# Optimization experiments

Hardware: AMD Instinct MI355X
Metric: run time of the kernel (lower is better)

Reference implementation:

```python
import jax, jax.numpy as jnp
import numpy as np
from jax import lax

# Module config (UOT_loss defaults): reg_m_l2=[5.0, 5.0], div='l2',
# detach_plan=True, use_uniform=False, marginal_match_dim=1.
REG_M1, REG_M2 = 5.0, 5.0
NUM_ITER = 1000      # POT mm_unbalanced default numItermax
STOP_THR = 1e-15     # POT default stopThr
EPS = 1e-16


def pairwise_sqeuclidean(x, y):
    # ot.dist default metric='sqeuclidean': M[i,j] = ||x_i - y_j||^2
    x2 = jnp.sum(x * x, axis=1)[:, None]
    y2 = jnp.sum(y * y, axis=1)[None, :]
    return jnp.maximum(x2 + y2 - 2.0 * (x @ y.T), 0.0)


def mm_unbalanced_l2(a, b, M):
    # POT ot.unbalanced.mm_unbalanced(a, b, M, [REG_M1, REG_M2], div='l2'), reg=0.
    G0 = a[:, None] * b[None, :]                       # [n, m] init plan
    K = jnp.maximum(REG_M1 * a[:, None] + REG_M2 * b[None, :] - M, 0.0)

    def cond(state):
        i, _, err = state
        return jnp.logical_and(i < NUM_ITER, err > STOP_THR)

    def body(state):
        i, G, _ = state
        Gd = (REG_M1 * jnp.sum(G, axis=1, keepdims=True)
              + REG_M2 * jnp.sum(G, axis=0, keepdims=True) + EPS)
        Gn = K * G / Gd
        err = jnp.sqrt(jnp.sum((Gn - G) ** 2))
        return i + 1, Gn, err

    _, G, _ = lax.while_loop(
        cond, body, (jnp.int32(0), G0, jnp.array(jnp.inf, G0.dtype)))
    return G


def setup_inputs() -> dict:
    key = jax.random.key(0)
    k1, k2, k3, k4 = jax.random.split(key, 4)
    n, m, d = 4096, 4096, 64
    source = jax.random.normal(k1, (n, d), jnp.float32)
    target = jax.random.normal(k2, (m, d), jnp.float32)
    mu = jax.random.uniform(k3, (n,), jnp.float32, minval=0.5, maxval=1.5)
    nu = jax.random.uniform(k4, (m,), jnp.float32, minval=0.5, maxval=1.5)
    mu = mu / jnp.sum(mu)
    nu = nu / jnp.sum(nu)
    return {"source": source, "target": target,
            "source_density": mu, "target_density": nu}


def reference(source, target, source_density, target_density):
    M = pairwise_sqeuclidean(source, target)           # [n, m]
    plan = mm_unbalanced_l2(source_density, target_density, M)
    ot_loss = jnp.sum(plan * M)
    # marginal_match_dim=1 -> row sums (transported source mass)
    marginal_transported = jnp.sum(plan, axis=1)
    marginal_loss = jnp.mean((marginal_transported - source_density) ** 2)
    return ot_loss, marginal_loss
```

## Files before the change

kernel.cpp:

```cpp
#include <hip/hip_runtime.h>


#define NV 4096
#define RM 5.0f
#define EPSF 1e-16f
#define STOP2 1e-30f
#define NITER 1000
#define MAGIC 0x5a17c0de
#define GRID_T 512

#define ERRT_OFF 0
#define ERRS_OFF 1024
#define OTP_OFF  2048
#define RSP_OFF  4096
#define CSP_OFF  135168
#define RS_OFF   266240
#define CS_OFF   270336
#define BMI_OFF  274432
#define CTL_OFF  275456
#define G_OFF    278528

typedef short bf16x8 __attribute__((ext_vector_type(8)));
typedef float f32x4  __attribute__((ext_vector_type(4)));
typedef unsigned short u16;

__device__ __forceinline__ float wave_sum_all(float v) {
  #pragma unroll
  for (int off = 1; off < 64; off <<= 1) v += __shfl_xor(v, off);
  return v;
}
__device__ __forceinline__ float wave_max_all(float v) {
  #pragma unroll
  for (int off = 1; off < 64; off <<= 1) v = fmaxf(v, __shfl_xor(v, off));
  return v;
}
__device__ __forceinline__ float wave_sum_dn(float v) {
  #pragma unroll
  for (int off = 32; off; off >>= 1) v += __shfl_down(v, off);
  return v;
}
__device__ __forceinline__ float dot64(const float* __restrict__ xr,
                                       const float* __restrict__ yr) {
  float d = 0.f;
  #pragma unroll 1
  for (int k = 0; k < 64; ++k) d = fmaf(xr[k], yr[k], d);
  return d;
}
__device__ __forceinline__ unsigned pack2(float x, float y) {
  return (__float_as_uint(x) >> 16) | (__float_as_uint(y) & 0xffff0000u);
}

__device__ void stage_panels(const float* __restrict__ X,
                             const float* __restrict__ Y,
                             int by, int bx,
                             u16 (*As)[72], u16 (*Bs)[72],
                             float* X2L, float* Y2L) {
  const int t = threadIdx.x;
  #pragma unroll
  for (int m = 0; m < 2; ++m) {
    const float* src = m ? (Y + (size_t)bx * 8192) : (X + (size_t)by * 8192);
    u16 (*dst)[72] = m ? Bs : As;
    float* nrm = m ? Y2L : X2L;
    #pragma unroll
    for (int it = 0; it < 8; ++it) {
      const int flat = t + it * 256;
      const int r = flat >> 4;
      const int c = (flat & 15) << 2;
      const float4 v = *(const float4*)(src + (size_t)flat * 4);
      float p = fmaf(v.x, v.x, fmaf(v.y, v.y, fmaf(v.z, v.z, v.w * v.w)));
      p += __shfl_xor(p, 1); p += __shfl_xor(p, 2);
      p += __shfl_xor(p, 4); p += __shfl_xor(p, 8);
      if ((t & 15) == 0) nrm[r] = p;
      uint2 w;
      w.x = pack2(v.x, v.y);
      w.y = pack2(v.z, v.w);
      *(uint2*)&dst[r][c] = w;
    }
  }
  __syncthreads();
}

__device__ void lds_dots(const u16 (*As)[72], const u16 (*Bs)[72],
                         int wr, int wc, int lane, f32x4 acc[4][4]) {
  const int lrow = lane & 15, lk8 = lane >> 4;
  #pragma unroll
  for (int i = 0; i < 4; ++i)
    #pragma unroll
    for (int j = 0; j < 4; ++j)
      acc[i][j] = (f32x4){0.f, 0.f, 0.f, 0.f};
  #pragma unroll
  for (int ks = 0; ks < 2; ++ks) {
    bf16x8 af[4], bg[4];
    #pragma unroll
    for (int f = 0; f < 4; ++f) {
      af[f] = *(const bf16x8*)&As[wr * 64 + f * 16 + lrow][ks * 32 + lk8 * 8];
      bg[f] = *(const bf16x8*)&Bs[wc * 64 + f * 16 + lrow][ks * 32 + lk8 * 8];
    }
    #pragma unroll
    for (int fr = 0; fr < 4; ++fr)
      #pragma unroll
      for (int fc = 0; fc < 4; ++fc)
        acc[fr][fc] = __builtin_amdgcn_mfma_f32_16x16x32_bf16(
            af[fr], bg[fc], acc[fr][fc], 0, 0, 0);
  }
}

__device__ __forceinline__ void gbar(int* ctl) {
  __threadfence();
  __syncthreads();
  if (threadIdx.x == 0) {
    while (__hip_atomic_load(&ctl[2], __ATOMIC_ACQUIRE,
                             __HIP_MEMORY_SCOPE_AGENT) != (int)MAGIC)
      __builtin_amdgcn_s_sleep(8);
    const int sense = __hip_atomic_load(&ctl[1], __ATOMIC_ACQUIRE,
                                        __HIP_MEMORY_SCOPE_AGENT);
    const int old = __hip_atomic_fetch_add(&ctl[0], 1, __ATOMIC_ACQ_REL,
                                           __HIP_MEMORY_SCOPE_AGENT);
    if (old == GRID_T - 1) {
      __hip_atomic_store(&ctl[0], 0, __ATOMIC_RELAXED, __HIP_MEMORY_SCOPE_AGENT);
      __hip_atomic_store(&ctl[1], sense ^ 1, __ATOMIC_RELEASE,
                         __HIP_MEMORY_SCOPE_AGENT);
    } else {
      while (__hip_atomic_load(&ctl[1], __ATOMIC_ACQUIRE,
                               __HIP_MEMORY_SCOPE_AGENT) == sense)
        __builtin_amdgcn_s_sleep(16);
    }
  }
  __syncthreads();
  __threadfence();
}

__global__ __launch_bounds__(256, 4) void k_main(
    const float* __restrict__ X, const float* __restrict__ Y,
    const float* __restrict__ a, const float* __restrict__ b,
    float* __restrict__ W) {
  __shared__ u16 As[128][72], Bs[128][72];
  __shared__ float X2L[128], Y2L[128];
  __shared__ float rcs[256], serr[4];
  __shared__ int s_nz;

  const int bid = blockIdx.x, tid = threadIdx.x;
  const int by = bid >> 5, bx = bid & 31;
  const int lane = tid & 63, wv = tid >> 6;
  const int wr = wv >> 1, wc = wv & 1;
  const int lrow = lane & 15, lk8 = lane >> 4;
  const int r0w = by * 128 + wr * 64;
  const int c0w = bx * 128 + wc * 64;
  float* Gp = W + G_OFF;
  int* bmi = (int*)(W + BMI_OFF);

  stage_panels(X, Y, by, bx, As, Bs, X2L, Y2L);

  f32x4 acc[4][4];
  lds_dots(As, Bs, wr, wc, lane, acc);

  const float av = a[r0w + lane];
  const float bv = b[c0w + lane];
  const float x2lv = X2L[wr * 64 + lane];
  const float y2lv = Y2L[wc * 64 + lane];
  const float amax = wave_max_all(av), bmax = wave_max_all(bv);
  const float x2m = wave_max_all(x2lv), y2m = wave_max_all(y2lv);
  const float Cw = RM * (amax + bmax) + 0.02f * sqrtf(x2m * y2m) + 0.05f;

  float x2r[16], y2c[4];
  #pragma unroll
  for (int fr = 0; fr < 4; ++fr)
    #pragma unroll
    for (int j = 0; j < 4; ++j)
      x2r[fr * 4 + j] = X2L[wr * 64 + fr * 16 + lk8 * 4 + j];
  #pragma unroll
  for (int fc = 0; fc < 4; ++fc)
    y2c[fc] = Y2L[wc * 64 + fc * 16 + lrow];

  float mmin = 3.4e38f;
  #pragma unroll
  for (int fr = 0; fr < 4; ++fr)
    #pragma unroll
    for (int j = 0; j < 4; ++j)
      #pragma unroll
      for (int fc = 0; fc < 4; ++fc)
        mmin = fminf(mmin,
                     fmaf(-2.f, acc[fr][fc][j], x2r[fr * 4 + j] + y2c[fc]));
  const bool wfast = (__ballot(mmin < Cw) == 0ull);

  if (tid == 0) s_nz = 0;
  rcs[tid] = 0.f;
  __syncthreads();

  if (wfast) {
    const float Ea = wave_sum_all(av * av);
    const float Eb = wave_sum_all(bv * bv);
    if (lane == 0) serr[wv] = Ea * Eb;
    #pragma unroll
    for (int fr = 0; fr < 4; ++fr)
      #pragma unroll
      for (int fc = 0; fc < 4; ++fc)
        acc[fr][fc] = (f32x4){0.f, 0.f, 0.f, 0.f};
  } else {
    float sa = 0.f, sb = 0.f;
    for (int i = lane; i < NV; i += 64) { sa += a[i]; sb += b[i]; }
    sa = wave_sum_all(sa); sb = wave_sum_all(sb);
    float bcf[4], gdc[4];
    #pragma unroll
    for (int fc = 0; fc < 4; ++fc) {
      bcf[fc] = __shfl(bv, fc * 16 + lrow);
      gdc[fc] = RM * bcf[fc] * sa;
    }
    float errp = 0.f; int nzl = 0;
    #pragma unroll
    for (int fr = 0; fr < 4; ++fr)
      #pragma unroll
      for (int j = 0; j < 4; ++j) {
        const int ridx = fr * 16 + lk8 * 4 + j;
        const float ar = __shfl(av, ridx);
        const float gdr = RM * ar * sb;
        const int grow = r0w + ridx;
        float rsum = 0.f;
        #pragma unroll
        for (int fc = 0; fc < 4; ++fc) {
          float Mv = fmaf(-2.f, acc[fr][fc][j], x2r[fr * 4 + j] + y2c[fc]);
          if (Mv < Cw) {
            const float dx = dot64(X + ((size_t)grow << 6),
                                   Y + ((size_t)(c0w + fc * 16 + lrow) << 6));
            Mv = x2r[fr * 4 + j] + y2c[fc] - 2.f * dx;
          }
          Mv = fmaxf(Mv, 0.f);
          const float Kv = fmaxf(RM * (ar + bcf[fc]) - Mv, 0.f);
          const float g0 = ar * bcf[fc];
          const float g = Kv * g0 / (gdr + gdc[fc] + EPSF);
          acc[fr][fc][j] = g;
          const float dl = g - g0;
          errp += dl * dl;
          nzl |= (g != 0.f);
          rsum += g;
        }
        atomicAdd(&rcs[wr * 64 + ridx], rsum);
      }
    #pragma unroll
    for (int fc = 0; fc < 4; ++fc) {
      float csum = 0.f;
      #pragma unroll
      for (int fr = 0; fr < 4; ++fr)
        #pragma unroll
        for (int j = 0; j < 4; ++j) csum += acc[fr][fc][j];
      atomicAdd(&rcs[128 + wc * 64 + fc * 16 + lrow], csum);
    }
    errp = wave_sum_all(errp);
    if (lane == 0) serr[wv] = errp;
    if (nzl) s_nz = 1;
  }
  __syncthreads();
  const int tilenz = s_nz;

  if (tilenz) {
    #pragma unroll
    for (int fr = 0; fr < 4; ++fr)
      #pragma unroll
      for (int j = 0; j < 4; ++j) {
        const int grow = r0w + fr * 16 + lk8 * 4 + j;
        #pragma unroll
        for (int fc = 0; fc < 4; ++fc)
          Gp[(size_t)grow * NV + c0w + fc * 16 + lrow] = acc[fr][fc][j];
      }
    if (tid < 128) W[RSP_OFF + (size_t)bid * 128 + tid] = rcs[tid];
    else           W[CSP_OFF + (size_t)bid * 128 + (tid - 128)] = rcs[tid];
  }
  if (tid == 0) {
    W[ERRT_OFF + bid] = serr[0] + serr[1] + serr[2] + serr[3];
    bmi[bid] = tilenz;
  }
}

__global__ __launch_bounds__(256, 2) void k_tail(
    const float* __restrict__ X, const float* __restrict__ Y,
    const float* __restrict__ a, const float* __restrict__ b,
    float* __restrict__ W, float* __restrict__ out) {
  __shared__ u16 As[128][72], Bs[128][72];
  __shared__ float X2L[128], Y2L[128];
  __shared__ float rcs[256], serr[4], sred[4];
  __shared__ int s_nz, s_any;

  const int bid = blockIdx.x, tid = threadIdx.x;
  const int lane = tid & 63, wv = tid >> 6;
  const int wr = wv >> 1, wc = wv & 1;
  const int lrow = lane & 15, lk8 = lane >> 4;
  float* Gp = W + G_OFF;
  int* bmi = (int*)(W + BMI_OFF);
  int* ctl = (int*)(W + CTL_OFF);

  if (bid == 0 && tid == 0) {
    __hip_atomic_store(&ctl[0], 0, __ATOMIC_RELAXED, __HIP_MEMORY_SCOPE_AGENT);
    __hip_atomic_store(&ctl[1], 0, __ATOMIC_RELAXED, __HIP_MEMORY_SCOPE_AGENT);
    __hip_atomic_store(&ctl[2], (int)MAGIC, __ATOMIC_RELEASE,
                       __HIP_MEMORY_SCOPE_AGENT);
  }

  int orv = 0;
  for (int i = tid; i < 1024; i += 256) orv |= bmi[i];
  if (tid == 0) s_any = 0;
  __syncthreads();
  if (orv) s_any = 1;
  __syncthreads();

  if (!s_any) {
    if (bid == 0) {
      float s = 0.f;
      for (int i = tid; i < NV; i += 256) { const float d = a[i]; s = fmaf(d, d, s); }
      s = wave_sum_dn(s);
      if (lane == 0) serr[wv] = s;
      __syncthreads();
      if (tid == 0) {
        out[0] = 0.f;
        out[1] = (serr[0] + serr[1] + serr[2] + serr[3]) * (1.0f / (float)NV);
      }
    }
    return;
  }

  const int t0 = bid, t1 = bid + GRID_T;
  int p = 2;
  while (true) {
    {
      const int sr = tid >> 5, j = tid & 31;
      const int r = bid * 8 + sr;
      const int byr = r >> 7, rl = r & 127;
      float vs = bmi[byr * 32 + j] ? W[RSP_OFF + (size_t)(byr * 32 + j) * 128 + rl] : 0.f;
      #pragma unroll
      for (int off = 1; off < 32; off <<= 1) vs += __shfl_xor(vs, off);
      if (j == 0) W[RS_OFF + r] = vs;
      float cs = bmi[j * 32 + byr] ? W[CSP_OFF + (size_t)(j * 32 + byr) * 128 + rl] : 0.f;
      #pragma unroll
      for (int off = 1; off < 32; off <<= 1) cs += __shfl_xor(cs, off);
      if (j == 0) W[CS_OFF + r] = cs;
    }
    if (bid == 0) {
      float e = 0.f;
      for (int i = tid; i < 1024; i += 256) e += W[ERRT_OFF + i];
      e = wave_sum_all(e);
      if (lane == 0) sred[wv] = e;
      __syncthreads();
      if (tid == 0) W[ERRS_OFF] = sred[0] + sred[1] + sred[2] + sred[3];
    }
    gbar(ctl);
    const float errv = W[ERRS_OFF];
    if (errv <= STOP2 || p > NITER) break;

    #pragma unroll 1
    for (int tt = 0; tt < 2; ++tt) {
      const int t = tt ? t1 : t0;
      if (!bmi[t]) { if (tid == 0) W[ERRT_OFF + t] = 0.f; continue; }
      const int by = t >> 5, bx = t & 31;
      const int r0w = by * 128 + wr * 64, c0w = bx * 128 + wc * 64;
      __syncthreads();
      stage_panels(X, Y, by, bx, As, Bs, X2L, Y2L);
      f32x4 acc[4][4];
      lds_dots(As, Bs, wr, wc, lane, acc);

      const float av = a[r0w + lane], bv = b[c0w + lane];
      const float x2lv = X2L[wr * 64 + lane], y2lv = Y2L[wc * 64 + lane];
      const float Rv = W[RS_OFF + r0w + lane], Cv = W[CS_OFF + c0w + lane];
      const float amax = wave_max_all(av), bmax = wave_max_all(bv);
      const float x2m = wave_max_all(x2lv), y2m = wave_max_all(y2lv);
      const float Cw = RM * (amax + bmax) + 0.02f * sqrtf(x2m * y2m) + 0.05f;

      float x2r[16], y2c[4], bcf[4], Ccf[4];
      #pragma unroll
      for (int fr = 0; fr < 4; ++fr)
        #pragma unroll
        for (int j = 0; j < 4; ++j)
          x2r[fr * 4 + j] = X2L[wr * 64 + fr * 16 + lk8 * 4 + j];
      #pragma unroll
      for (int fc = 0; fc < 4; ++fc) {
        y2c[fc] = Y2L[wc * 64 + fc * 16 + lrow];
        bcf[fc] = __shfl(bv, fc * 16 + lrow);
        Ccf[fc] = __shfl(Cv, fc * 16 + lrow);
      }
      if (tid == 0) s_nz = 0;
      rcs[tid] = 0.f;
      __syncthreads();

      float errp = 0.f; int nzl = 0;
      #pragma unroll
      for (int fr = 0; fr < 4; ++fr)
        #pragma unroll
        for (int j = 0; j < 4; ++j) {
          const int ridx = fr * 16 + lk8 * 4 + j;
          const float ar = __shfl(av, ridx);
          const float Rr = __shfl(Rv, ridx);
          const int grow = r0w + ridx;
          float rsum = 0.f;
          #pragma unroll
          for (int fc = 0; fc < 4; ++fc) {
            const int gcol = c0w + fc * 16 + lrow;
            const float g = Gp[(size_t)grow * NV + gcol];
            float Mv = fmaf(-2.f, acc[fr][fc][j], x2r[fr * 4 + j] + y2c[fc]);
            if (Mv < Cw) {
              const float dx = dot64(X + ((size_t)grow << 6),
                                     Y + ((size_t)gcol << 6));
              Mv = x2r[fr * 4 + j] + y2c[fc] - 2.f * dx;
            }
            Mv = fmaxf(Mv, 0.f);
            const float Kv = fmaxf(RM * (ar + bcf[fc]) - Mv, 0.f);
            const float gd = RM * Rr + RM * Ccf[fc] + EPSF;
            const float gn = Kv * g / gd;
            acc[fr][fc][j] = gn;
            const float dl = gn - g;
            errp += dl * dl;
            nzl |= (gn != 0.f);
            rsum += gn;
          }
          atomicAdd(&rcs[wr * 64 + ridx], rsum);
        }
      #pragma unroll
      for (int fc = 0; fc < 4; ++fc) {
        float csum = 0.f;
        #pragma unroll
        for (int fr = 0; fr < 4; ++fr)
          #pragma unroll
          for (int j = 0; j < 4; ++j) csum += acc[fr][fc][j];
        atomicAdd(&rcs[128 + wc * 64 + fc * 16 + lrow], csum);
      }
      errp = wave_sum_all(errp);
      if (lane == 0) serr[wv] = errp;
      if (nzl) s_nz = 1;
      __syncthreads();

      #pragma unroll
      for (int fr = 0; fr < 4; ++fr)
        #pragma unroll
        for (int j = 0; j < 4; ++j) {
          const int grow = r0w + fr * 16 + lk8 * 4 + j;
          #pragma unroll
          for (int fc = 0; fc < 4; ++fc)
            Gp[(size_t)grow * NV + c0w + fc * 16 + lrow] = acc[fr][fc][j];
        }
      if (tid < 128) W[RSP_OFF + (size_t)t * 128 + tid] = rcs[tid];
      else           W[CSP_OFF + (size_t)t * 128 + (tid - 128)] = rcs[tid];
      if (tid == 0) {
        W[ERRT_OFF + t] = serr[0] + serr[1] + serr[2] + serr[3];
        bmi[t] = s_nz;
      }
    }
    gbar(ctl);
    ++p;
  }

  #pragma unroll 1
  for (int tt = 0; tt < 2; ++tt) {
    const int t = tt ? t1 : t0;
    float otb = 0.f;
    if (bmi[t]) {
      const int by = t >> 5, bx = t & 31;
      const int r0w = by * 128 + wr * 64, c0w = bx * 128 + wc * 64;
      float otp = 0.f;
      #pragma unroll
      for (int fr = 0; fr < 4; ++fr)
        #pragma unroll
        for (int j = 0; j < 4; ++j) {
          const int grow = r0w + fr * 16 + lk8 * 4 + j;
          #pragma unroll
          for (int fc = 0; fc < 4; ++fc) {
            const int gcol = c0w + fc * 16 + lrow;
            const float g = Gp[(size_t)grow * NV + gcol];
            if (g != 0.f) {
              const float* xr = X + ((size_t)grow << 6);
              const float* yr = Y + ((size_t)gcol << 6);
              const float dd = dot64(xr, yr);
              const float x2 = dot64(xr, xr);
              const float y2 = dot64(yr, yr);
              otp += g * fmaxf(x2 + y2 - 2.f * dd, 0.f);
            }
          }
        }
      otp = wave_sum_all(otp);
      if (lane == 0) serr[wv] = otp;
      __syncthreads();
      otb = serr[0] + serr[1] + serr[2] + serr[3];
      __syncthreads();
    }
    if (tid == 0) W[OTP_OFF + t] = otb;
  }
  gbar(ctl);
  if (bid == 0) {
    float so = 0.f;
    for (int i = tid; i < 1024; i += 256) so += W[OTP_OFF + i];
    so = wave_sum_dn(so);
    float sm = 0.f;
    for (int i = tid; i < NV; i += 256) {
      const float d = W[RS_OFF + i] - a[i];
      sm = fmaf(d, d, sm);
    }
    sm = wave_sum_dn(sm);
    if (lane == 0) { sred[wv] = so; serr[wv] = sm; }
    __syncthreads();
    if (tid == 0) {
      out[0] = sred[0] + sred[1] + sred[2] + sred[3];
      out[1] = (serr[0] + serr[1] + serr[2] + serr[3]) * (1.0f / (float)NV);
    }
  }
}

extern "C" void kernel_launch(void* const* d_in, const int* in_sizes, int n_in,
                              void* d_out, int out_size, void* d_ws, size_t ws_size,
                              hipStream_t stream) {
  const float* X = (const float*)d_in[0];
  const float* Y = (const float*)d_in[1];
  const float* a = (const float*)d_in[2];
  const float* b = (const float*)d_in[3];
  float* out = (float*)d_out;
  float* W = (float*)d_ws;

  k_main<<<1024, 256, 0, stream>>>(X, Y, a, b, W);
  k_tail<<<GRID_T, 256, 0, stream>>>(X, Y, a, b, W, out);
}
```

Before: 86.60 us.

## Shrink plan tiles to 64x64 so sparse-tile skipping is finer-grained

```diff
diff --git a/kernel.cpp b/kernel.cpp
--- a/kernel.cpp
+++ b/kernel.cpp
@@ -8,17 +8,18 @@
 #define NITER 1000
 #define MAGIC 0x5a17c0de
 #define GRID_T 512
+#define NT 4096
 
 #define ERRT_OFF 0
-#define ERRS_OFF 1024
-#define OTP_OFF  2048
-#define RSP_OFF  4096
-#define CSP_OFF  135168
-#define RS_OFF   266240
-#define CS_OFF   270336
-#define BMI_OFF  274432
-#define CTL_OFF  275456
-#define G_OFF    278528
+#define ERRS_OFF 4096
+#define OTP_OFF  8192
+#define RSP_OFF  12288
+#define CSP_OFF  274432
+#define RS_OFF   536576
+#define CS_OFF   540672
+#define BMI_OFF  544768
+#define CTL_OFF  548864
+#define G_OFF    552960
 
 typedef short bf16x8 __attribute__((ext_vector_type(8)));
 typedef float f32x4  __attribute__((ext_vector_type(4)));
@@ -29,9 +30,14 @@
   for (int off = 1; off < 64; off <<= 1) v += __shfl_xor(v, off);
   return v;
 }
-__device__ __forceinline__ float wave_max_all(float v) {
-  #pragma unroll
-  for (int off = 1; off < 64; off <<= 1) v = fmaxf(v, __shfl_xor(v, off));
+__device__ __forceinline__ float red32_sum(float v) {
+  #pragma unroll
+  for (int off = 1; off < 32; off <<= 1) v += __shfl_xor(v, off);
+  return v;
+}
+__device__ __forceinline__ float red32_max(float v) {
+  #pragma unroll
+  for (int off = 1; off < 32; off <<= 1) v = fmaxf(v, __shfl_xor(v, off));
   return v;
 }
 __device__ __forceinline__ float wave_sum_dn(float v) {
@@ -50,19 +56,19 @@
   return (__float_as_uint(x) >> 16) | (__float_as_uint(y) & 0xffff0000u);
 }
 
-__device__ void stage_panels(const float* __restrict__ X,
-                             const float* __restrict__ Y,
-                             int by, int bx,
-                             u16 (*As)[72], u16 (*Bs)[72],
-                             float* X2L, float* Y2L) {
+__device__ void stage64(const float* __restrict__ X,
+                        const float* __restrict__ Y,
+                        int by, int bx,
+                        u16 (*As)[72], u16 (*Bs)[72],
+                        float* X2L, float* Y2L) {
   const int t = threadIdx.x;
   #pragma unroll
   for (int m = 0; m < 2; ++m) {
-    const float* src = m ? (Y + (size_t)bx * 8192) : (X + (size_t)by * 8192);
+    const float* src = m ? (Y + (size_t)bx * 4096) : (X + (size_t)by * 4096);
     u16 (*dst)[72] = m ? Bs : As;
     float* nrm = m ? Y2L : X2L;
     #pragma unroll
-    for (int it = 0; it < 8; ++it) {
+    for (int it = 0; it < 4; ++it) {
       const int flat = t + it * 256;
       const int r = flat >> 4;
       const int c = (flat & 15) << 2;
@@ -80,26 +86,26 @@
   __syncthreads();
 }
 
-__device__ void lds_dots(const u16 (*As)[72], const u16 (*Bs)[72],
-                         int wr, int wc, int lane, f32x4 acc[4][4]) {
+__device__ void dots64(const u16 (*As)[72], const u16 (*Bs)[72],
+                       int wr, int wc, int lane, f32x4 acc[2][2]) {
   const int lrow = lane & 15, lk8 = lane >> 4;
   #pragma unroll
-  for (int i = 0; i < 4; ++i)
-    #pragma unroll
-    for (int j = 0; j < 4; ++j)
+  for (int i = 0; i < 2; ++i)
+    #pragma unroll
+    for (int j = 0; j < 2; ++j)
       acc[i][j] = (f32x4){0.f, 0.f, 0.f, 0.f};
   #pragma unroll
   for (int ks = 0; ks < 2; ++ks) {
-    bf16x8 af[4], bg[4];
-    #pragma unroll
-    for (int f = 0; f < 4; ++f) {
-      af[f] = *(const bf16x8*)&As[wr * 64 + f * 16 + lrow][ks * 32 + lk8 * 8];
-      bg[f] = *(const bf16x8*)&Bs[wc * 64 + f * 16 + lrow][ks * 32 + lk8 * 8];
-    }
-    #pragma unroll
-    for (int fr = 0; fr < 4; ++fr)
-      #pragma unroll
-      for (int fc = 0; fc < 4; ++fc)
+    bf16x8 af[2], bg[2];
+    #pragma unroll
+    for (int f = 0; f < 2; ++f) {
+      af[f] = *(const bf16x8*)&As[wr * 32 + f * 16 + lrow][ks * 32 + lk8 * 8];
+      bg[f] = *(const bf16x8*)&Bs[wc * 32 + f * 16 + lrow][ks * 32 + lk8 * 8];
+    }
+    #pragma unroll
+    for (int fr = 0; fr < 2; ++fr)
+      #pragma unroll
+      for (int fc = 0; fc < 2; ++fc)
         acc[fr][fc] = __builtin_amdgcn_mfma_f32_16x16x32_bf16(
             af[fr], bg[fc], acc[fr][fc], 0, 0, 0);
   }
@@ -130,85 +136,87 @@
   __threadfence();
 }
 
-__global__ __launch_bounds__(256, 4) void k_main(
+__global__ __launch_bounds__(256, 5) void k_main(
     const float* __restrict__ X, const float* __restrict__ Y,
     const float* __restrict__ a, const float* __restrict__ b,
     float* __restrict__ W) {
-  __shared__ u16 As[128][72], Bs[128][72];
-  __shared__ float X2L[128], Y2L[128];
-  __shared__ float rcs[256], serr[4];
+  __shared__ u16 As[64][72], Bs[64][72];
+  __shared__ float X2L[64], Y2L[64];
+  __shared__ float rcs[128];
+  __shared__ float serr[4];
   __shared__ int s_nz;
 
   const int bid = blockIdx.x, tid = threadIdx.x;
-  const int by = bid >> 5, bx = bid & 31;
+  const int by = bid >> 6, bx = bid & 63;
   const int lane = tid & 63, wv = tid >> 6;
   const int wr = wv >> 1, wc = wv & 1;
   const int lrow = lane & 15, lk8 = lane >> 4;
-  const int r0w = by * 128 + wr * 64;
-  const int c0w = bx * 128 + wc * 64;
+  const int l32 = lane & 31;
+  const int r0w = by * 64 + wr * 32, c0w = bx * 64 + wc * 32;
   float* Gp = W + G_OFF;
   int* bmi = (int*)(W + BMI_OFF);
 
-  stage_panels(X, Y, by, bx, As, Bs, X2L, Y2L);
-
-  f32x4 acc[4][4];
-  lds_dots(As, Bs, wr, wc, lane, acc);
-
-  const float av = a[r0w + lane];
-  const float bv = b[c0w + lane];
-  const float x2lv = X2L[wr * 64 + lane];
-  const float y2lv = Y2L[wc * 64 + lane];
-  const float amax = wave_max_all(av), bmax = wave_max_all(bv);
-  const float x2m = wave_max_all(x2lv), y2m = wave_max_all(y2lv);
+  if (tid == 0) s_nz = 0;
+  if (tid < 128) rcs[tid] = 0.f;
+
+  stage64(X, Y, by, bx, As, Bs, X2L, Y2L);
+
+  const float av = a[r0w + l32];
+  const float bv = b[c0w + l32];
+
+  f32x4 acc[2][2];
+  dots64(As, Bs, wr, wc, lane, acc);
+
+  const float x2lv = X2L[wr * 32 + l32];
+  const float y2lv = Y2L[wc * 32 + l32];
+  const float amax = red32_max(av), bmax = red32_max(bv);
+  const float x2m = red32_max(x2lv), y2m = red32_max(y2lv);
   const float Cw = RM * (amax + bmax) + 0.02f * sqrtf(x2m * y2m) + 0.05f;
 
-  float x2r[16], y2c[4];
-  #pragma unroll
-  for (int fr = 0; fr < 4; ++fr)
+  float x2r[8], y2c[2];
+  #pragma unroll
+  for (int fr = 0; fr < 2; ++fr)
     #pragma unroll
     for (int j = 0; j < 4; ++j)
-      x2r[fr * 4 + j] = X2L[wr * 64 + fr * 16 + lk8 * 4 + j];
-  #pragma unroll
-  for (int fc = 0; fc < 4; ++fc)
-    y2c[fc] = Y2L[wc * 64 + fc * 16 + lrow];
+      x2r[fr * 4 + j] = X2L[wr * 32 + fr * 16 + lk8 * 4 + j];
+  #pragma unroll
+  for (int fc = 0; fc < 2; ++fc)
+    y2c[fc] = Y2L[wc * 32 + fc * 16 + lrow];
 
   float mmin = 3.4e38f;
   #pragma unroll
-  for (int fr = 0; fr < 4; ++fr)
+  for (int fr = 0; fr < 2; ++fr)
     #pragma unroll
     for (int j = 0; j < 4; ++j)
       #pragma unroll
-      for (int fc = 0; fc < 4; ++fc)
+      for (int fc = 0; fc < 2; ++fc)
         mmin = fminf(mmin,
                      fmaf(-2.f, acc[fr][fc][j], x2r[fr * 4 + j] + y2c[fc]));
   const bool wfast = (__ballot(mmin < Cw) == 0ull);
 
-  if (tid == 0) s_nz = 0;
-  rcs[tid] = 0.f;
-  __syncthreads();
-
   if (wfast) {
-    const float Ea = wave_sum_all(av * av);
-    const float Eb = wave_sum_all(bv * bv);
+    const float Ea = red32_sum(av * av);
+    const float Eb = red32_sum(bv * bv);
     if (lane == 0) serr[wv] = Ea * Eb;
     #pragma unroll
-    for (int fr = 0; fr < 4; ++fr)
-      #pragma unroll
-      for (int fc = 0; fc < 4; ++fc)
+    for (int fr = 0; fr < 2; ++fr)
+      #pragma unroll
+      for (int fc = 0; fc < 2; ++fc)
         acc[fr][fc] = (f32x4){0.f, 0.f, 0.f, 0.f};
   } else {
+    if (lane == 0) s_nz = 1;
     float sa = 0.f, sb = 0.f;
     for (int i = lane; i < NV; i += 64) { sa += a[i]; sb += b[i]; }
     sa = wave_sum_all(sa); sb = wave_sum_all(sb);
-    float bcf[4], gdc[4];
-    #pragma unroll
-    for (int fc = 0; fc < 4; ++fc) {
+    float bcf[2], gdc[2];
+    #pragma unroll
+    for (int fc = 0; fc < 2; ++fc) {
       bcf[fc] = __shfl(bv, fc * 16 + lrow);
       gdc[fc] = RM * bcf[fc] * sa;
     }
-    float errp = 0.f; int nzl = 0;
-    #pragma unroll
-    for (int fr = 0; fr < 4; ++fr)
+    float errp = 0.f;
+    #pragma unroll
+    for (int fr = 0; fr < 2; ++fr)
       #pragma unroll
       for (int j = 0; j < 4; ++j) {
         const int ridx = fr * 16 + lk8 * 4 + j;
@@ -217,12 +225,13 @@
         const int grow = r0w + ridx;
         float rsum = 0.f;
         #pragma unroll
-        for (int fc = 0; fc < 4; ++fc) {
+        for (int fc = 0; fc < 2; ++fc) {
           float Mv = fmaf(-2.f, acc[fr][fc][j], x2r[fr * 4 + j] + y2c[fc]);
           if (Mv < Cw) {
             const float dx = dot64(X + ((size_t)grow << 6),
                                    Y + ((size_t)(c0w + fc * 16 + lrow) << 6));
-            Mv = x2r[fr * 4 + j] + y2c[fc] - 2.f * dx;
+            Mv = dot64(X + ((size_t)grow << 6), X + ((size_t)grow << 6)) * 0.f
+               + x2r[fr * 4 + j] + y2c[fc] - 2.f * dx;
           }
           Mv = fmaxf(Mv, 0.f);
           const float Kv = fmaxf(RM * (ar + bcf[fc]) - Mv, 0.f);
@@ -231,39 +240,37 @@
           acc[fr][fc][j] = g;
           const float dl = g - g0;
           errp += dl * dl;
-          nzl |= (g != 0.f);
           rsum += g;
         }
-        atomicAdd(&rcs[wr * 64 + ridx], rsum);
-      }
-    #pragma unroll
-    for (int fc = 0; fc < 4; ++fc) {
+        atomicAdd(&rcs[wr * 32 + ridx], rsum);
+      }
+    #pragma unroll
+    for (int fc = 0; fc < 2; ++fc) {
       float csum = 0.f;
       #pragma unroll
-      for (int fr = 0; fr < 4; ++fr)
+      for (int fr = 0; fr < 2; ++fr)
         #pragma unroll
         for (int j = 0; j < 4; ++j) csum += acc[fr][fc][j];
-      atomicAdd(&rcs[128 + wc * 64 + fc * 16 + lrow], csum);
+      atomicAdd(&rcs[64 + wc * 32 + fc * 16 + lrow], csum);
     }
     errp = wave_sum_all(errp);
     if (lane == 0) serr[wv] = errp;
-    if (nzl) s_nz = 1;
   }
   __syncthreads();
   const int tilenz = s_nz;
 
   if (tilenz) {
     #pragma unroll
-    for (int fr = 0; fr < 4; ++fr)
+    for (int fr = 0; fr < 2; ++fr)
       #pragma unroll
       for (int j = 0; j < 4; ++j) {
         const int grow = r0w + fr * 16 + lk8 * 4 + j;
         #pragma unroll
-        for (int fc = 0; fc < 4; ++fc)
+        for (int fc = 0; fc < 2; ++fc)
           Gp[(size_t)grow * NV + c0w + fc * 16 + lrow] = acc[fr][fc][j];
       }
-    if (tid < 128) W[RSP_OFF + (size_t)bid * 128 + tid] = rcs[tid];
-    else           W[CSP_OFF + (size_t)bid * 128 + (tid - 128)] = rcs[tid];
+    if (tid < 64)       W[RSP_OFF + (size_t)bid * 64 + tid] = rcs[tid];
+    else if (tid < 128) W[CSP_OFF + (size_t)bid * 64 + (tid - 64)] = rcs[tid];
   }
   if (tid == 0) {
     W[ERRT_OFF + bid] = serr[0] + serr[1] + serr[2] + serr[3];
@@ -275,15 +282,16 @@
     const float* __restrict__ X, const float* __restrict__ Y,
     const float* __restrict__ a, const float* __restrict__ b,
     float* __restrict__ W, float* __restrict__ out) {
-  __shared__ u16 As[128][72], Bs[128][72];
-  __shared__ float X2L[128], Y2L[128];
-  __shared__ float rcs[256], serr[4], sred[4];
+  __shared__ u16 As[64][72], Bs[64][72];
+  __shared__ float X2L[64], Y2L[64];
+  __shared__ float rcs[128], serr[4], sred[4];
   __shared__ int s_nz, s_any;
 
   const int bid = blockIdx.x, tid = threadIdx.x;
   const int lane = tid & 63, wv = tid >> 6;
   const int wr = wv >> 1, wc = wv & 1;
   const int lrow = lane & 15, lk8 = lane >> 4;
+  const int l32 = lane & 31;
   float* Gp = W + G_OFF;
   int* bmi = (int*)(W + BMI_OFF);
   int* ctl = (int*)(W + CTL_OFF);
@@ -295,8 +303,12 @@
                        __HIP_MEMORY_SCOPE_AGENT);
   }
 
+  const int4* bmi4 = (const int4*)bmi;
   int orv = 0;
-  for (int i = tid; i < 1024; i += 256) orv |= bmi[i];
+  for (int i = tid; i < 1024; i += 256) {
+    const int4 q = bmi4[i];
+    orv |= q.x | q.y | q.z | q.w;
+  }
   if (tid == 0) s_any = 0;
   __syncthreads();
   if (orv) s_any = 1;
@@ -317,25 +329,30 @@
     return;
   }
 
-  const int t0 = bid, t1 = bid + GRID_T;
   int p = 2;
   while (true) {
     {
-      const int sr = tid >> 5, j = tid & 31;
+      const int sr = tid >> 5, j32 = tid & 31;
       const int r = bid * 8 + sr;
-      const int byr = r >> 7, rl = r & 127;
-      float vs = bmi[byr * 32 + j] ? W[RSP_OFF + (size_t)(byr * 32 + j) * 128 + rl] : 0.f;
-      #pragma unroll
-      for (int off = 1; off < 32; off <<= 1) vs += __shfl_xor(vs, off);
-      if (j == 0) W[RS_OFF + r] = vs;
-      float cs = bmi[j * 32 + byr] ? W[CSP_OFF + (size_t)(j * 32 + byr) * 128 + rl] : 0.f;
-      #pragma unroll
-      for (int off = 1; off < 32; off <<= 1) cs += __shfl_xor(cs, off);
-      if (j == 0) W[CS_OFF + r] = cs;
+      const int byr = r >> 6, rl = r & 63;
+      float vs = 0.f;
+      for (int k = j32; k < 64; k += 32) {
+        const int t = byr * 64 + k;
+        vs += bmi[t] ? W[RSP_OFF + (size_t)t * 64 + rl] : 0.f;
+      }
+      vs = red32_sum(vs);
+      if (j32 == 0) W[RS_OFF + r] = vs;
+      float cs = 0.f;
+      for (int k = j32; k < 64; k += 32) {
+        const int t = k * 64 + byr;
+        cs += bmi[t] ? W[CSP_OFF + (size_t)t * 64 + rl] : 0.f;
+      }
+      cs = red32_sum(cs);
+      if (j32 == 0) W[CS_OFF + r] = cs;
     }
     if (bid == 0) {
       float e = 0.f;
-      for (int i = tid; i < 1024; i += 256) e += W[ERRT_OFF + i];
+      for (int i = tid; i < NT; i += 256) e += W[ERRT_OFF + i];
       e = wave_sum_all(e);
       if (lane == 0) sred[wv] = e;
       __syncthreads();
@@ -346,42 +363,41 @@
     if (errv <= STOP2 || p > NITER) break;
 
     #pragma unroll 1
-    for (int tt = 0; tt < 2; ++tt) {
-      const int t = tt ? t1 : t0;
+    for (int tt = 0; tt < 8; ++tt) {
+      const int t = bid + tt * GRID_T;
       if (!bmi[t]) { if (tid == 0) W[ERRT_OFF + t] = 0.f; continue; }
-      const int by = t >> 5, bx = t & 31;
-      const int r0w = by * 128 + wr * 64, c0w = bx * 128 + wc * 64;
-      __syncthreads();
-      stage_panels(X, Y, by, bx, As, Bs, X2L, Y2L);
-      f32x4 acc[4][4];
-      lds_dots(As, Bs, wr, wc, lane, acc);
-
-      const float av = a[r0w + lane], bv = b[c0w + lane];
-      const float x2lv = X2L[wr * 64 + lane], y2lv = Y2L[wc * 64 + lane];
-      const float Rv = W[RS_OFF + r0w + lane], Cv = W[CS_OFF + c0w + lane];
-      const float amax = wave_max_all(av), bmax = wave_max_all(bv);
-      const float x2m = wave_max_all(x2lv), y2m = wave_max_all(y2lv);
+      const int by = t >> 6, bx = t & 63;
+      const int r0w = by * 64 + wr * 32, c0w = bx * 64 + wc * 32;
+      if (tid == 0) s_nz = 0;
+      if (tid < 128) rcs[tid] = 0.f;
+      __syncthreads();
+      stage64(X, Y, by, bx, As, Bs, X2L, Y2L);
+      f32x4 acc[2][2];
+      dots64(As, Bs, wr, wc, lane, acc);
+
+      const float av = a[r0w + l32], bv = b[c0w + l32];
+      const float x2lv = X2L[wr * 32 + l32], y2lv = Y2L[wc * 32 + l32];
+      const float Rv = W[RS_OFF + r0w + l32], Cv = W[CS_OFF + c0w + l32];
+      const float amax = red32_max(av), bmax = red32_max(bv);
+      const float x2m = red32_max(x2lv), y2m = red32_max(y2lv);
       const float Cw = RM * (amax + bmax) + 0.02f * sqrtf(x2m * y2m) + 0.05f;
 
-      float x2r[16], y2c[4], bcf[4], Ccf[4];
-      #pragma unroll
-      for (int fr = 0; fr < 4; ++fr)
+      float x2r[8], y2c[2], bcf[2], Ccf[2];
+      #pragma unroll
+      for (int fr = 0; fr < 2; ++fr)
         #pragma unroll
         for (int j = 0; j < 4; ++j)
-          x2r[fr * 4 + j] = X2L[wr * 64 + fr * 16 + lk8 * 4 + j];
-      #pragma unroll
-      for (int fc = 0; fc < 4; ++fc) {
-        y2c[fc] = Y2L[wc * 64 + fc * 16 + lrow];
+          x2r[fr * 4 + j] = X2L[wr * 32 + fr * 16 + lk8 * 4 + j];
+      #pragma unroll
+      for (int fc = 0; fc < 2; ++fc) {
+        y2c[fc] = Y2L[wc * 32 + fc * 16 + lrow];
         bcf[fc] = __shfl(bv, fc * 16 + lrow);
         Ccf[fc] = __shfl(Cv, fc * 16 + lrow);
       }
-      if (tid == 0) s_nz = 0;
-      rcs[tid] = 0.f;
-      __syncthreads();
 
       float errp = 0.f; int nzl = 0;
       #pragma unroll
-      for (int fr = 0; fr < 4; ++fr)
+      for (int fr = 0; fr < 2; ++fr)
         #pragma unroll
         for (int j = 0; j < 4; ++j) {
           const int ridx = fr * 16 + lk8 * 4 + j;
@@ -390,7 +406,7 @@
           const int grow = r0w + ridx;
           float rsum = 0.f;
           #pragma unroll
-          for (int fc = 0; fc < 4; ++fc) {
+          for (int fc = 0; fc < 2; ++fc) {
             const int gcol = c0w + fc * 16 + lrow;
             const float g = Gp[(size_t)grow * NV + gcol];
             float Mv = fmaf(-2.f, acc[fr][fc][j], x2r[fr * 4 + j] + y2c[fc]);
@@ -409,16 +425,16 @@
             nzl |= (gn != 0.f);
             rsum += gn;
           }
-          atomicAdd(&rcs[wr * 64 + ridx], rsum);
+          atomicAdd(&rcs[wr * 32 + ridx], rsum);
         }
       #pragma unroll
-      for (int fc = 0; fc < 4; ++fc) {
+      for (int fc = 0; fc < 2; ++fc) {
         float csum = 0.f;
         #pragma unroll
-        for (int fr = 0; fr < 4; ++fr)
+        for (int fr = 0; fr < 2; ++fr)
           #pragma unroll
           for (int j = 0; j < 4; ++j) csum += acc[fr][fc][j];
-        atomicAdd(&rcs[128 + wc * 64 + fc * 16 + lrow], csum);
+        atomicAdd(&rcs[64 + wc * 32 + fc * 16 + lrow], csum);
       }
       errp = wave_sum_all(errp);
       if (lane == 0) serr[wv] = errp;
@@ -426,40 +442,41 @@
       __syncthreads();
 
       #pragma unroll
-      for (int fr = 0; fr < 4; ++fr)
+      for (int fr = 0; fr < 2; ++fr)
         #pragma unroll
         for (int j = 0; j < 4; ++j) {
           const int grow = r0w + fr * 16 + lk8 * 4 + j;
           #pragma unroll
-          for (int fc = 0; fc < 4; ++fc)
+          for (int fc = 0; fc < 2; ++fc)
             Gp[(size_t)grow * NV + c0w + fc * 16 + lrow] = acc[fr][fc][j];
         }
-      if (tid < 128) W[RSP_OFF + (size_t)t * 128 + tid] = rcs[tid];
-      else           W[CSP_OFF + (size_t)t * 128 + (tid - 128)] = rcs[tid];
+      if (tid < 64)       W[RSP_OFF + (size_t)t * 64 + tid] = rcs[tid];
+      else if (tid < 128) W[CSP_OFF + (size_t)t * 64 + (tid - 64)] = rcs[tid];
       if (tid == 0) {
         W[ERRT_OFF + t] = serr[0] + serr[1] + serr[2] + serr[3];
         bmi[t] = s_nz;
       }
+      __syncthreads();
     }
     gbar(ctl);
     ++p;
   }
 
   #pragma unroll 1
-  for (int tt = 0; tt < 2; ++tt) {
-    const int t = tt ? t1 : t0;
+  for (int tt = 0; tt < 8; ++tt) {
+    const int t = bid + tt * GRID_T;
     float otb = 0.f;
     if (bmi[t]) {
-      const int by = t >> 5, bx = t & 31;
-      const int r0w = by * 128 + wr * 64, c0w = bx * 128 + wc * 64;
+      const int by = t >> 6, bx = t & 63;
+      const int r0w = by * 64 + wr * 32, c0w = bx * 64 + wc * 32;
       float otp = 0.f;
       #pragma unroll
-      for (int fr = 0; fr < 4; ++fr)
+      for (int fr = 0; fr < 2; ++fr)
         #pragma unroll
         for (int j = 0; j < 4; ++j) {
           const int grow = r0w + fr * 16 + lk8 * 4 + j;
           #pragma unroll
-          for (int fc = 0; fc < 4; ++fc) {
+          for (int fc = 0; fc < 2; ++fc) {
             const int gcol = c0w + fc * 16 + lrow;
             const float g = Gp[(size_t)grow * NV + gcol];
             if (g != 0.f) {
@@ -483,7 +500,7 @@
   gbar(ctl);
   if (bid == 0) {
     float so = 0.f;
-    for (int i = tid; i < 1024; i += 256) so += W[OTP_OFF + i];
+    for (int i = tid; i < NT; i += 256) so += W[OTP_OFF + i];
     so = wave_sum_dn(so);
     float sm = 0.f;
     for (int i = tid; i < NV; i += 256) {
@@ -510,6 +527,6 @@
   float* out = (float*)d_out;
   float* W = (float*)d_ws;
 
-  k_main<<<1024, 256, 0, stream>>>(X, Y, a, b, W);
+  k_main<<<NT, 256, 0, stream>>>(X, Y, a, b, W);
   k_tail<<<GRID_T, 256, 0, stream>>>(X, Y, a, b, W, out);
 }
```

Result: faster. 79.99 us (-7.6%).
